# Optimization experiments

Hardware: AMD Instinct MI355X
Metric: run time of the kernel (lower is better)

The kernel has to match this reference:

```python
import jax, jax.numpy as jnp
import numpy as np

B, IN_C, OUT_C, K, H, W = 8, 256, 256, 3, 128, 128
EPS = 1e-8
ACT_SCALE = np.sqrt(2.0).astype(np.float32)


def setup_inputs() -> dict:
    key = jax.random.key(0)
    k1, k2, k3 = jax.random.split(key, 3)
    return {
        "x": jax.random.normal(k1, (B, IN_C, H, W), dtype=jnp.float32),
        "code": jax.random.normal(k2, (B, IN_C), dtype=jnp.float32),
        "weight": jax.random.normal(k3, (OUT_C, IN_C, K, K), dtype=jnp.float32),
        "bias": jnp.zeros((OUT_C,), dtype=jnp.float32),
    }


def reference(x, code, weight, bias):
    b, in_c, h, w = x.shape
    out_c, _, k, _ = weight.shape
    wscale = np.float32(1.0 / np.sqrt(k * k * in_c))
    # Same memory reinterpretation as torch .view: (out_c,in_c,k,k) -> (1,k,k,in_c,out_c)
    wv = (weight * wscale).reshape(1, k, k, in_c, out_c)
    # modulate per-sample by code over input channels
    wm = wv * code[:, None, None, :, None]            # [b,k,k,in_c,out_c]
    # demodulate: norm over (k,k,in_c) per (b,out_c)
    norm = jnp.sqrt(jnp.sum(wm * wm, axis=(1, 2, 3)) + EPS)  # [b,out_c]
    wm = wm / norm[:, None, None, None, :]
    # reshape to grouped-conv kernel [b*out_c, in_c, k, k]
    wk = jnp.transpose(wm, (0, 4, 3, 1, 2)).reshape(b * out_c, in_c, k, k)
    xg = x.reshape(1, b * in_c, h, w)
    y = jax.lax.conv_general_dilated(
        xg, wk, window_strides=(1, 1),
        padding=[(k // 2, k // 2), (k // 2, k // 2)],
        feature_group_count=b,
        dimension_numbers=("NCHW", "OIHW", "NCHW"))
    y = y.reshape(b, out_c, h, w) + bias[None, :, None, None]
    # LeakyReLU(0.2) * sqrt(2)
    return jnp.where(y >= 0, y, 0.2 * y) * ACT_SCALE
```

## Files before the change

### kernel.cpp

```cpp
#include <hip/hip_runtime.h>
#include <hip/hip_bf16.h>


typedef __attribute__((ext_vector_type(8))) short short8;
typedef __attribute__((ext_vector_type(4))) float floatx4;
typedef __bf16 bf16x8 __attribute__((ext_vector_type(8)));

#define B_    8
#define IC_   256
#define OC_   256
#define HW_   128
#define PIX_  (HW_*HW_)
#define RTOT  2304
#define WSCALE (1.0f/48.0f)

#define SWZ(row) ((((row) >> 1) & 3) << 3)

static __device__ __forceinline__ floatx4 mfma_bf16(short8 a, short8 b, floatx4 c) {
  return __builtin_amdgcn_mfma_f32_16x16x32_bf16(
      __builtin_bit_cast(bf16x8, a), __builtin_bit_cast(bf16x8, b), c, 0, 0, 0);
}

static __device__ __forceinline__ unsigned short f2bf(float f) {
  unsigned int u = __builtin_bit_cast(unsigned int, f);
  return (unsigned short)(u >> 16) + (unsigned short)((u >> 15) & 1u);
}

__global__ __launch_bounds__(256) void k_zero(float* __restrict__ p, int n) {
  int i = blockIdx.x * 256 + threadIdx.x;
  if (i < n) p[i] = 0.f;
}

__global__ __launch_bounds__(256) void k_norm(const float* __restrict__ Wraw,
                                              const float* __restrict__ code,
                                              float* __restrict__ norm2) {
  const int tap = blockIdx.x % 9, b = blockIdx.x / 9;
  const int oc = threadIdx.x;
  __shared__ float cs[IC_];
  cs[oc] = code[b * IC_ + oc];
  __syncthreads();
  float s = 0.f;
#pragma unroll 8
  for (int ic = 0; ic < IC_; ++ic) {
    float v = Wraw[(size_t)(tap * IC_ + ic) * OC_ + oc] * cs[ic];
    s += v * v;
  }
  atomicAdd(&norm2[b * OC_ + oc], s * (WSCALE * WSCALE));
}

__global__ __launch_bounds__(256) void k_modw(const float* __restrict__ Wraw,
                                              const float* __restrict__ code,
                                              const float* __restrict__ norm2,
                                              unsigned short* __restrict__ Wt) {
  const int idx = blockIdx.x * 256 + threadIdx.x;
  const int r  = idx % RTOT;
  const int t2 = idx / RTOT;
  const int oc = t2 & 255;
  const int b  = t2 >> 8;
  const int ic = r & 255;
  const float w  = Wraw[(size_t)r * OC_ + oc];
  const float cd = code[b * IC_ + ic];
  const float rn = rsqrtf(norm2[b * OC_ + oc] + 1e-8f);
  Wt[idx] = f2bf(w * cd * WSCALE * rn);
}

__global__ __launch_bounds__(256, 2) void k_conv(const float* __restrict__ x,
                                                 const unsigned short* __restrict__ Wt,
                                                 const float* __restrict__ bias,
                                                 float* __restrict__ out) {
  __shared__ __align__(16) unsigned short Wl[2][3][128 * 32];
  __shared__ __align__(16) unsigned short Xl[2][130 * 32];

  const int tid  = threadIdx.x;
  const int lane = tid & 63;
  const int wv   = tid >> 6;
  const int wm   = wv & 1;
  const int wn   = wv >> 1;
  const int l15  = lane & 15;
  const int k0   = (lane >> 4) * 8;

  const int nwg  = (int)(gridDim.x * gridDim.y * gridDim.z);
  const int q    = nwg >> 3;
  const int flat = (int)(blockIdx.x + gridDim.x * (blockIdx.y + gridDim.y * blockIdx.z));
  const int nf   = (flat & 7) * q + (flat >> 3);
  const int py = nf & 127, ot = (nf >> 7) & 1, b = nf >> 8;

  const unsigned short* Wtp = Wt + (size_t)(b * OC_ + ot * 128) * RTOT;
  const float* xb = x + (size_t)b * IC_ * PIX_;

  const int srow = tid >> 1;
  const int xh   = tid & 1;
  const int sW   = SWZ(srow);
  const int sX   = SWZ(srow + 1);
  const int eW0  = (xh * 16) ^ sW;
  const int eX0  = (xh * 16) ^ sX;

  const int sA  = SWZ(l15);
  const int sB0 = SWZ(l15), sB1 = SWZ(l15 + 1), sB2 = SWZ(l15 + 2);

  const int lo = (py > 0) ? py - 1 : 0;
  const int hi = (py < HW_ - 1) ? py + 1 : HW_ - 1;
  const int NS = (hi - lo + 1) * 8;

  const floatx4 zz = {0.f, 0.f, 0.f, 0.f};
  floatx4 acc[4][4];
#pragma unroll
  for (int i = 0; i < 4; ++i)
#pragma unroll
    for (int j = 0; j < 4; ++j) acc[i][j] = zz;

  if (tid < 128) {
    const int bi = tid >> 6, rr = tid & 63;
    const int r = (rr < 32) ? 0 : 129;
    Xl[bi][r * 32 + (rr & 31)] = 0;
  }

  float xr[16];
  short8 wr0, wr1, wr2, wr3, wr4, wr5;

#define CLOAD(s_) do {                                                           \
    const int iy_   = lo + ((s_) >> 3);                                          \
    const int icc_  = (s_) & 7;                                                  \
    const int tapb_ = (iy_ - py + 1) * 3;                                        \
    const float* xs_ = xb + (size_t)(icc_ * 32 + xh * 16) * PIX_ + iy_ * HW_ + srow; \
    _Pragma("unroll")                                                            \
    for (int i_ = 0; i_ < 16; ++i_) xr[i_] = xs_[(size_t)i_ * PIX_];             \
    const unsigned short* ws_ =                                                  \
        Wtp + (size_t)srow * RTOT + (size_t)tapb_ * IC_ + icc_ * 32 + xh * 16;   \
    wr0 = *(const short8*)(ws_);                                                 \
    wr1 = *(const short8*)(ws_ + 8);                                             \
    wr2 = *(const short8*)(ws_ + IC_);                                           \
    wr3 = *(const short8*)(ws_ + IC_ + 8);                                       \
    wr4 = *(const short8*)(ws_ + 2 * IC_);                                       \
    wr5 = *(const short8*)(ws_ + 2 * IC_ + 8);                                   \
  } while (0)

#define DSW(b_) do {                                                             \
    short8 p0_, p1_;                                                             \
    _Pragma("unroll")                                                            \
    for (int c_ = 0; c_ < 8; ++c_) {                                             \
      p0_[c_] = (short)f2bf(xr[c_]);                                             \
      p1_[c_] = (short)f2bf(xr[8 + c_]);                                         \
    }                                                                            \
    unsigned short* xd_ = &Xl[b_][(srow + 1) * 32];                              \
    *(short8*)(&xd_[eX0])     = p0_;                                             \
    *(short8*)(&xd_[eX0 ^ 8]) = p1_;                                             \
    unsigned short* wd0_ = &Wl[b_][0][srow * 32];                                \
    unsigned short* wd1_ = &Wl[b_][1][srow * 32];                                \
    unsigned short* wd2_ = &Wl[b_][2][srow * 32];                                \
    *(short8*)(&wd0_[eW0])     = wr0;                                            \
    *(short8*)(&wd0_[eW0 ^ 8]) = wr1;                                            \
    *(short8*)(&wd1_[eW0])     = wr2;                                            \
    *(short8*)(&wd1_[eW0 ^ 8]) = wr3;                                            \
    *(short8*)(&wd2_[eW0])     = wr4;                                            \
    *(short8*)(&wd2_[eW0 ^ 8]) = wr5;                                            \
  } while (0)

  CLOAD(0);
  DSW(0);
  __syncthreads();

  for (int s = 0; s < NS; ++s) {
    const int nb = s & 1;
    if (s + 1 < NS) CLOAD(s + 1);

    __builtin_amdgcn_s_setprio(1);
#pragma unroll
    for (int kx = 0; kx < 3; ++kx) {
      const int sB = (kx == 0) ? sB0 : (kx == 1) ? sB1 : sB2;
      short8 af[4], bfr[4];
#pragma unroll
      for (int i = 0; i < 4; ++i)
        af[i] = *(const short8*)(&Wl[nb][kx][(wm * 64 + i * 16 + l15) * 32 + (k0 ^ sA)]);
#pragma unroll
      for (int j = 0; j < 4; ++j)
        bfr[j] = *(const short8*)(&Xl[nb][(wn * 64 + j * 16 + l15 + kx) * 32 + (k0 ^ sB)]);
#pragma unroll
      for (int i = 0; i < 4; ++i)
#pragma unroll
        for (int j = 0; j < 4; ++j)
          acc[i][j] = mfma_bf16(af[i], bfr[j], acc[i][j]);
    }
    __builtin_amdgcn_s_setprio(0);

    if (s + 1 < NS) DSW(nb ^ 1);
    __syncthreads();
  }

#undef CLOAD
#undef DSW

  const int row0 = (lane >> 4) * 4;
#pragma unroll
  for (int i = 0; i < 4; ++i) {
#pragma unroll
    for (int p = 0; p < 4; ++p) {
      const int oc = ot * 128 + wm * 64 + i * 16 + row0 + p;
      const float bvf = bias[oc];
#pragma unroll
      for (int j = 0; j < 4; ++j) {
        const int px = wn * 64 + j * 16 + l15;
        float v = acc[i][j][p] + bvf;
        v = (v >= 0.f ? v : 0.2f * v) * 1.41421356237f;
        out[((size_t)(b * OC_ + oc) * HW_ + py) * HW_ + px] = v;
      }
    }
  }
}

extern "C" void kernel_launch(void* const* d_in, const int* in_sizes, int n_in,
                              void* d_out, int out_size, void* d_ws, size_t ws_size,
                              hipStream_t stream) {
  const float* x    = (const float*)d_in[0];
  const float* code = (const float*)d_in[1];
  const float* wgt  = (const float*)d_in[2];
  const float* bias = (const float*)d_in[3];

  const size_t WT_BYTES = (size_t)B_ * OC_ * RTOT * 2;

  unsigned short* Wt = (unsigned short*)d_ws;
  float* norm2       = (float*)((char*)d_ws + WT_BYTES);

  k_zero<<<(B_ * OC_ + 255) / 256, 256, 0, stream>>>(norm2, B_ * OC_);
  k_norm<<<B_ * 9, 256, 0, stream>>>(wgt, code, norm2);
  k_modw<<<(B_ * OC_ * RTOT) / 256, 256, 0, stream>>>(wgt, code, norm2, Wt);
  k_conv<<<dim3(HW_, 2, B_), 256, 0, stream>>>(x, Wt, bias, (float*)d_out);
}
```

Measured before the change: 466.8 us.

## Pre-swizzle modulated weights into MFMA fragment layout and load directly to registers

The weight-modulation kernel now writes bf16 weights in a layout that matches the MFMA A-fragment, so the conv kernel loads them straight from global memory into registers instead of staging them through LDS. This removes the weight LDS buffers, their stores and reads, and the bank-swizzle logic. The main loop is unrolled by two with separate register sets for alternating stages, and block ordering is changed so the two output-channel halves of a row are adjacent. The cost is many more vector registers (24 short8 for weights plus 32 floats for x), which risks spills or lower occupancy, and each wave now fetches weights from global or L2 memory without sharing them through LDS.

```diff
diff --git a/kernel.cpp b/kernel.cpp
--- a/kernel.cpp
+++ b/kernel.cpp
@@ -13,6 +13,7 @@
 #define PIX_  (HW_*HW_)
 #define RTOT  2304
 #define WSCALE (1.0f/48.0f)
+#define WT2_PER_B (RTOT * OC_)
 
 #define SWZ(row) ((((row) >> 1) & 3) << 3)
 
@@ -51,24 +52,28 @@
 __global__ __launch_bounds__(256) void k_modw(const float* __restrict__ Wraw,
                                               const float* __restrict__ code,
                                               const float* __restrict__ norm2,
-                                              unsigned short* __restrict__ Wt) {
+                                              unsigned short* __restrict__ Wt2) {
   const int idx = blockIdx.x * 256 + threadIdx.x;
-  const int r  = idx % RTOT;
-  const int t2 = idx / RTOT;
-  const int oc = t2 & 255;
-  const int b  = t2 >> 8;
-  const int ic = r & 255;
-  const float w  = Wraw[(size_t)r * OC_ + oc];
+  const int e   = idx & 7;
+  const int l15 = (idx >> 3) & 15;
+  const int kg  = (idx >> 7) & 3;
+  const int og  = (idx >> 9) & 15;
+  const int icc = (idx >> 13) & 7;
+  const int bt  = idx >> 16;
+  const int b   = bt / 9;
+  const int tap = bt - b * 9;
+  const int oc  = og * 16 + l15;
+  const int ic  = icc * 32 + kg * 8 + e;
+  const float w  = Wraw[(size_t)(tap * IC_ + ic) * OC_ + oc];
   const float cd = code[b * IC_ + ic];
   const float rn = rsqrtf(norm2[b * OC_ + oc] + 1e-8f);
-  Wt[idx] = f2bf(w * cd * WSCALE * rn);
+  Wt2[idx] = f2bf(w * cd * WSCALE * rn);
 }
 
 __global__ __launch_bounds__(256, 2) void k_conv(const float* __restrict__ x,
-                                                 const unsigned short* __restrict__ Wt,
+                                                 const unsigned short* __restrict__ Wt2,
                                                  const float* __restrict__ bias,
                                                  float* __restrict__ out) {
-  __shared__ __align__(16) unsigned short Wl[2][3][128 * 32];
   __shared__ __align__(16) unsigned short Xl[2][130 * 32];
 
   const int tid  = threadIdx.x;
@@ -83,19 +88,19 @@
   const int q    = nwg >> 3;
   const int flat = (int)(blockIdx.x + gridDim.x * (blockIdx.y + gridDim.y * blockIdx.z));
   const int nf   = (flat & 7) * q + (flat >> 3);
-  const int py = nf & 127, ot = (nf >> 7) & 1, b = nf >> 8;
-
-  const unsigned short* Wtp = Wt + (size_t)(b * OC_ + ot * 128) * RTOT;
+  const int ot = nf & 1, py = (nf >> 1) & 127, b = nf >> 8;
+
+  const unsigned short* wb2 = Wt2 + (size_t)b * WT2_PER_B;
   const float* xb = x + (size_t)b * IC_ * PIX_;
 
   const int srow = tid >> 1;
   const int xh   = tid & 1;
-  const int sW   = SWZ(srow);
   const int sX   = SWZ(srow + 1);
-  const int eW0  = (xh * 16) ^ sW;
   const int eX0  = (xh * 16) ^ sX;
 
-  const int sA  = SWZ(l15);
+  const int ogb  = ot * 8 + wm * 4;
+  const int wlo  = lane * 8;
+
   const int sB0 = SWZ(l15), sB1 = SWZ(l15 + 1), sB2 = SWZ(l15 + 2);
 
   const int lo = (py > 0) ? py - 1 : 0;
@@ -115,80 +120,85 @@
     Xl[bi][r * 32 + (rr & 31)] = 0;
   }
 
-  float xr[16];
-  short8 wr0, wr1, wr2, wr3, wr4, wr5;
-
-#define CLOAD(s_) do {                                                           \
-    const int iy_   = lo + ((s_) >> 3);                                          \
-    const int icc_  = (s_) & 7;                                                  \
+  float xrA[16], xrB[16];
+  short8 wA[12], wB[12];
+
+#define XL(t_, XR_) do { if ((t_) < NS) {                                        \
+    const int iy_  = lo + ((t_) >> 3);                                           \
+    const int icc_ = (t_) & 7;                                                   \
+    const float* xs_ = xb + (size_t)(icc_ * 32 + xh * 16) * PIX_ + iy_ * HW_ + srow; \
+    _Pragma("unroll")                                                            \
+    for (int i_ = 0; i_ < 16; ++i_) XR_[i_] = xs_[(size_t)i_ * PIX_];            \
+  } } while (0)
+
+#define WL(t_, W_) do { if ((t_) < NS) {                                         \
+    const int iy_   = lo + ((t_) >> 3);                                          \
+    const int icc_  = (t_) & 7;                                                  \
     const int tapb_ = (iy_ - py + 1) * 3;                                        \
-    const float* xs_ = xb + (size_t)(icc_ * 32 + xh * 16) * PIX_ + iy_ * HW_ + srow; \
-    _Pragma("unroll")                                                            \
-    for (int i_ = 0; i_ < 16; ++i_) xr[i_] = xs_[(size_t)i_ * PIX_];             \
-    const unsigned short* ws_ =                                                  \
-        Wtp + (size_t)srow * RTOT + (size_t)tapb_ * IC_ + icc_ * 32 + xh * 16;   \
-    wr0 = *(const short8*)(ws_);                                                 \
-    wr1 = *(const short8*)(ws_ + 8);                                             \
-    wr2 = *(const short8*)(ws_ + IC_);                                           \
-    wr3 = *(const short8*)(ws_ + IC_ + 8);                                       \
-    wr4 = *(const short8*)(ws_ + 2 * IC_);                                       \
-    wr5 = *(const short8*)(ws_ + 2 * IC_ + 8);                                   \
-  } while (0)
-
-#define DSW(b_) do {                                                             \
+    _Pragma("unroll")                                                            \
+    for (int kx_ = 0; kx_ < 3; ++kx_) {                                          \
+      const unsigned short* p_ =                                                 \
+          wb2 + ((size_t)(((tapb_ + kx_) * 8 + icc_) * 16 + ogb) << 9) + wlo;    \
+      _Pragma("unroll")                                                          \
+      for (int i_ = 0; i_ < 4; ++i_)                                             \
+        W_[kx_ * 4 + i_] = *(const short8*)(p_ + i_ * 512);                      \
+    }                                                                            \
+  } } while (0)
+
+#define DSW(t_, XR_) do { if ((t_) < NS) {                                       \
     short8 p0_, p1_;                                                             \
     _Pragma("unroll")                                                            \
     for (int c_ = 0; c_ < 8; ++c_) {                                             \
-      p0_[c_] = (short)f2bf(xr[c_]);                                             \
-      p1_[c_] = (short)f2bf(xr[8 + c_]);                                         \
+      p0_[c_] = (short)f2bf(XR_[c_]);                                            \
+      p1_[c_] = (short)f2bf(XR_[8 + c_]);                                        \
     }                                                                            \
-    unsigned short* xd_ = &Xl[b_][(srow + 1) * 32];                              \
+    unsigned short* xd_ = &Xl[(t_) & 1][(srow + 1) * 32];                        \
     *(short8*)(&xd_[eX0])     = p0_;                                             \
     *(short8*)(&xd_[eX0 ^ 8]) = p1_;                                             \
-    unsigned short* wd0_ = &Wl[b_][0][srow * 32];                                \
-    unsigned short* wd1_ = &Wl[b_][1][srow * 32];                                \
-    unsigned short* wd2_ = &Wl[b_][2][srow * 32];                                \
-    *(short8*)(&wd0_[eW0])     = wr0;                                            \
-    *(short8*)(&wd0_[eW0 ^ 8]) = wr1;                                            \
-    *(short8*)(&wd1_[eW0])     = wr2;                                            \
-    *(short8*)(&wd1_[eW0 ^ 8]) = wr3;                                            \
-    *(short8*)(&wd2_[eW0])     = wr4;                                            \
-    *(short8*)(&wd2_[eW0 ^ 8]) = wr5;                                            \
+  } } while (0)
+
+#define MM(nb_, W_) do {                                                         \
+    __builtin_amdgcn_s_setprio(1);                                               \
+    _Pragma("unroll")                                                            \
+    for (int kx_ = 0; kx_ < 3; ++kx_) {                                          \
+      const int sB_ = (kx_ == 0) ? sB0 : (kx_ == 1) ? sB1 : sB2;                 \
+      short8 bfr_[4];                                                            \
+      _Pragma("unroll")                                                          \
+      for (int j_ = 0; j_ < 4; ++j_)                                             \
+        bfr_[j_] = *(const short8*)(                                             \
+            &Xl[nb_][(wn * 64 + j_ * 16 + l15 + kx_) * 32 + (k0 ^ sB_)]);        \
+      _Pragma("unroll")                                                          \
+      for (int i_ = 0; i_ < 4; ++i_)                                             \
+        _Pragma("unroll")                                                        \
+        for (int j_ = 0; j_ < 4; ++j_)                                           \
+          acc[i_][j_] = mfma_bf16(W_[kx_ * 4 + i_], bfr_[j_], acc[i_][j_]);      \
+    }                                                                            \
+    __builtin_amdgcn_s_setprio(0);                                               \
   } while (0)
 
-  CLOAD(0);
-  DSW(0);
+  XL(0, xrA);
+  XL(1, xrB);
+  WL(0, wA);
+  DSW(0, xrA);
   __syncthreads();
 
-  for (int s = 0; s < NS; ++s) {
-    const int nb = s & 1;
-    if (s + 1 < NS) CLOAD(s + 1);
-
-    __builtin_amdgcn_s_setprio(1);
-#pragma unroll
-    for (int kx = 0; kx < 3; ++kx) {
-      const int sB = (kx == 0) ? sB0 : (kx == 1) ? sB1 : sB2;
-      short8 af[4], bfr[4];
-#pragma unroll
-      for (int i = 0; i < 4; ++i)
-        af[i] = *(const short8*)(&Wl[nb][kx][(wm * 64 + i * 16 + l15) * 32 + (k0 ^ sA)]);
-#pragma unroll
-      for (int j = 0; j < 4; ++j)
-        bfr[j] = *(const short8*)(&Xl[nb][(wn * 64 + j * 16 + l15 + kx) * 32 + (k0 ^ sB)]);
-#pragma unroll
-      for (int i = 0; i < 4; ++i)
-#pragma unroll
-        for (int j = 0; j < 4; ++j)
-          acc[i][j] = mfma_bf16(af[i], bfr[j], acc[i][j]);
-    }
-    __builtin_amdgcn_s_setprio(0);
-
-    if (s + 1 < NS) DSW(nb ^ 1);
+  for (int s = 0; s < NS; s += 2) {
+    XL(s + 2, xrA);
+    WL(s + 1, wB);
+    MM(0, wA);
+    DSW(s + 1, xrB);
     __syncthreads();
-  }
-
-#undef CLOAD
+    XL(s + 3, xrB);
+    WL(s + 2, wA);
+    MM(1, wB);
+    DSW(s + 2, xrA);
+    __syncthreads();
+  }
+
+#undef XL
+#undef WL
 #undef DSW
+#undef MM
 
   const int row0 = (lane >> 4) * 4;
 #pragma unroll
@@ -216,13 +226,13 @@
   const float* wgt  = (const float*)d_in[2];
   const float* bias = (const float*)d_in[3];
 
-  const size_t WT_BYTES = (size_t)B_ * OC_ * RTOT * 2;
-
-  unsigned short* Wt = (unsigned short*)d_ws;
-  float* norm2       = (float*)((char*)d_ws + WT_BYTES);
+  const size_t WT_BYTES = (size_t)B_ * WT2_PER_B * 2;
+
+  unsigned short* Wt2 = (unsigned short*)d_ws;
+  float* norm2        = (float*)((char*)d_ws + WT_BYTES);
 
   k_zero<<<(B_ * OC_ + 255) / 256, 256, 0, stream>>>(norm2, B_ * OC_);
   k_norm<<<B_ * 9, 256, 0, stream>>>(wgt, code, norm2);
-  k_modw<<<(B_ * OC_ * RTOT) / 256, 256, 0, stream>>>(wgt, code, norm2, Wt);
-  k_conv<<<dim3(HW_, 2, B_), 256, 0, stream>>>(x, Wt, bias, (float*)d_out);
-}
+  k_modw<<<(B_ * WT2_PER_B) / 256, 256, 0, stream>>>(wgt, code, norm2, Wt2);
+  k_conv<<<dim3(HW_, 2, B_), 256, 0, stream>>>(x, Wt2, bias, (float*)d_out);
+}
```

Result: faster. 441.3 us (-5.5%).
